# Performance work log

Hardware: AMD Instinct MI355X
Metric: run time of the kernel (lower is better)

Reference implementation:

```python
import jax, jax.numpy as jnp
import numpy as np

# config constants (from init_kwargs)
IMG_W = 800
IMG_H = 320
NUM_POINTS = 72
N_STRIPS = NUM_POINTS - 1
MAX_LANES = 4
REFINE_LAYERS = 3
CLS_W, REG_W, IOU_W = 2.0, 0.5, 2.0
ALPHA_NEG, ALPHA_POS, GAMMA = 0.1, 0.9, 2.0
LIOU_LEN = 15.0


def setup_inputs() -> dict:
    key = jax.random.key(0)
    k1, k2, k3, k4 = jax.random.split(key, 4)
    S, B, N, L, D = REFINE_LAYERS, 32, 2000, MAX_LANES, 2 + 4 + NUM_POINTS
    pred_fir = jax.random.uniform(k1, (S, B, N, D), dtype=jnp.float32)
    pred_sec = jax.random.uniform(k2, (S, B, N, D), dtype=jnp.float32)
    gt = jax.random.uniform(k3, (B, L, D), dtype=jnp.float32)
    gt = gt.at[..., 1].set(1.0)                    # all lanes valid
    # target offsets live in pixel coords; let some fall outside [0, IMG_W) to exercise invalid mask
    gt = gt.at[..., 6:].set(gt[..., 6:] * (IMG_W * 1.1) - 0.05 * IMG_W)
    diff = jax.random.uniform(k4, (S, N), dtype=jnp.float32)
    return {"predictions_fir": pred_fir, "predictions_sec": pred_sec,
            "gt_lane": gt, "diff": diff}


def _greedy_assign(cost):
    # cost: [N, L] -> matched prior row per target column, greedy without replacement
    N = cost.shape[0]
    def body(used, col):
        c = jnp.where(used, jnp.inf, col)
        r = jnp.argmin(c)
        return used.at[r].set(True), r
    _, rows = jax.lax.scan(body, jnp.zeros((N,), bool), cost.T)
    return rows  # [L] int32


def _assign_all(preds, gt):
    # preds: [S,B,N,D], gt: [B,L,D]; matching is under no_grad in the original
    p = jax.lax.stop_gradient(preds)
    t = jax.lax.stop_gradient(gt)
    score = jax.nn.softmax(p[..., :2], axis=-1)[..., 1]            # [S,B,N]
    geo = jnp.abs(p[..., :, None, 2:6] - t[None, :, None, :, 2:6]).sum(-1)   # [S,B,N,L]
    off = jnp.abs(p[..., :, None, 6:] - t[None, :, None, :, 6:] / (IMG_W - 1)).mean(-1)
    cost = geo + off - score[..., None]                            # [S,B,N,L]
    S, B, N, L = cost.shape
    rows = jax.vmap(_greedy_assign)(cost.reshape(S * B, N, L))
    return rows.reshape(S, B, L)


def _smooth_l1(d):
    ad = jnp.abs(d)
    return jnp.where(ad < 1.0, 0.5 * d * d, ad - 0.5)


def _branch_loss(preds, gt):
    # preds: [S,B,N,D], gt: [B,L,D] -> instance loss [N], last matched rows [L]
    S, B, N, _ = preds.shape
    L = gt.shape[1]
    rows = _assign_all(preds, gt)                                  # [S,B,L]

    # focal cls loss, per prior, summed over stages & batch
    cls_t = jax.nn.one_hot(rows, N, dtype=preds.dtype).sum(2)      # [S,B,N] 0/1
    logp = jax.nn.log_softmax(preds[..., :2], axis=-1)
    logpt = jnp.where(cls_t > 0, logp[..., 1], logp[..., 0])
    pt = jnp.exp(logpt)
    alpha_t = jnp.where(cls_t > 0, ALPHA_POS, ALPHA_NEG)
    cls_loss = (-alpha_t * (1.0 - pt) ** GAMMA * logpt).sum((0, 1)) / (B * REFINE_LAYERS)  # [N]

    # gather matched priors: [S,B,L,D]
    pm = jnp.take_along_axis(preds, rows[..., None], axis=2)
    tgt = gt[None]                                                 # [1,B,L,D]

    # smooth-L1 on (y, x, theta, length)
    sc = jnp.array([N_STRIPS, IMG_W - 1, 180.0, N_STRIPS], preds.dtype)
    d = pm[..., 2:6] * sc - tgt[..., 2:6] * sc
    reg_loss = (_smooth_l1(d).mean(-1) / L).sum((0, 1)) / (B * REFINE_LAYERS)  # [L]

    # line IoU loss on offsets
    rp = pm[..., 6:] * (IMG_W - 1)
    rt = jnp.broadcast_to(tgt[..., 6:], rp.shape)
    invalid = (rt < 0) | (rt >= IMG_W)
    ovr = jnp.minimum(rp + LIOU_LEN, rt + LIOU_LEN) - jnp.maximum(rp - LIOU_LEN, rt - LIOU_LEN)
    uni = jnp.maximum(rp + LIOU_LEN, rt + LIOU_LEN) - jnp.minimum(rp - LIOU_LEN, rt - LIOU_LEN)
    ovr = jnp.where(invalid, 0.0, ovr)
    uni = jnp.where(invalid, 0.0, uni)
    iou = ovr.sum(-1) / (uni.sum(-1) + 1e-9)                       # [S,B,L]
    iou_loss = ((1.0 - iou) / L).sum((0, 1)) / (B * REFINE_LAYERS) # [L]

    inst = cls_loss * CLS_W
    rows_last = rows[-1, -1]                                       # last stage, last image
    inst = inst.at[rows_last].add(reg_loss * REG_W + iou_loss * IOU_W)
    return inst


def reference(predictions_fir, predictions_sec, gt_lane, diff):
    loss_A = _branch_loss(predictions_fir, gt_lane)   # [N]
    loss_B = _branch_loss(predictions_sec, gt_lane)   # [N]
    diff_mean = diff.mean(0)                          # [N]
    delta = jax.lax.stop_gradient(jnp.median(loss_A - loss_B))
    loss_A = loss_A - delta / 2
    loss_B = loss_B + delta / 2
    total = jnp.sum((1.0 - diff_mean) * loss_A + diff_mean * loss_B)
    return total
```

## Files before the change

### kernel.cpp

```cpp
#include <hip/hip_runtime.h>
#include <math.h>

#define SDIM 3
#define BDIM 32
#define NPRI 2000
#define LDIM 4
#define DDIM 78
#define NOFF 72
#define NSB (SDIM * BDIM)
#define CHUNK 128
#define NCHUNK 16


__global__ __launch_bounds__(256) void prep_kernel(
    const float* __restrict__ gt, float* __restrict__ tgdiv,
    float* __restrict__ clsSum, float* __restrict__ corrws,
    float* __restrict__ regacc)
{
    int tid = blockIdx.x * 256 + threadIdx.x;
    if (tid < BDIM * 36 * 8) {
        int b = tid / 288, r = tid % 288, jj = r / 8, t = r % 8;
        int l = t >> 1, k = t & 1;
        tgdiv[tid] = gt[((size_t)b * LDIM + l) * DDIM + 6 + 2 * jj + k] / 799.0f;
    }
    if (tid < 2 * NPRI) { clsSum[tid] = 0.0f; corrws[tid] = 0.0f; }
    if (tid < 16) regacc[tid] = 0.0f;
}

__global__ __launch_bounds__(256) void cost_kernel(
    const float* __restrict__ predsA, const float* __restrict__ predsB,
    const float* __restrict__ gt, const float* __restrict__ tgdiv,
    float* __restrict__ costws, float* __restrict__ clsSum)
{
    const int chunk = blockIdx.x;
    const int sb = blockIdx.y;
    const int branch = blockIdx.z;
    const float* preds = branch ? predsB : predsA;
    const int bimg = sb % BDIM;
    const int tid = threadIdx.x;
    const int base_n = chunk * CHUNK;
    const int ntile = min(CHUNK, NPRI - base_n);

    __shared__ float tile[CHUNK * DDIM];

    {
        const float4* src = (const float4*)(preds + ((size_t)sb * NPRI + base_n) * DDIM);
        float4* dst = (float4*)tile;
        const int nf4 = ntile * DDIM / 4;
        for (int k = tid; k < nf4; k += 256) dst[k] = src[k];
    }
    __syncthreads();

    const int wv = tid >> 6, lane = tid & 63;
    const int i = wv * 32 + (lane >> 1);
    const int h = lane & 1;
    if (i >= ntile) return;
    const int n = base_n + i;
    const float* p = &tile[i * DDIM];

    const float* gtb = gt + (size_t)bimg * LDIM * DDIM;
    const float* tgb = tgdiv + (size_t)bimg * 288;

    float offs0 = 0.f, offs1 = 0.f, offs2 = 0.f, offs3 = 0.f;
    const int jj0 = h * 18;
#pragma unroll 6
    for (int jj = jj0; jj < jj0 + 18; ++jj) {
        float pv0 = p[6 + 2 * jj];
        float pv1 = p[7 + 2 * jj];
        const float* t8 = tgb + jj * 8;
        offs0 += fabsf(pv0 - t8[0]); offs0 += fabsf(pv1 - t8[1]);
        offs1 += fabsf(pv0 - t8[2]); offs1 += fabsf(pv1 - t8[3]);
        offs2 += fabsf(pv0 - t8[4]); offs2 += fabsf(pv1 - t8[5]);
        offs3 += fabsf(pv0 - t8[6]); offs3 += fabsf(pv1 - t8[7]);
    }
    offs0 += __shfl_xor(offs0, 1);
    offs1 += __shfl_xor(offs1, 1);
    offs2 += __shfl_xor(offs2, 1);
    offs3 += __shfl_xor(offs3, 1);

    if (h == 0) {
        float a = p[0], b1 = p[1];
        float m = fmaxf(a, b1);
        float ea = expf(a - m), eb = expf(b1 - m);
        float score = eb / (ea + eb);
        float g0 = p[2], g1 = p[3], g2 = p[4], g3 = p[5];
        float offs[4] = {offs0, offs1, offs2, offs3};
        float* cw = costws + ((size_t)(branch * NSB + sb) * LDIM) * NPRI + n;
#pragma unroll
        for (int l = 0; l < LDIM; ++l) {
            float geo = fabsf(g0 - gtb[l * DDIM + 2]) + fabsf(g1 - gtb[l * DDIM + 3])
                      + fabsf(g2 - gtb[l * DDIM + 4]) + fabsf(g3 - gtb[l * DDIM + 5]);
            cw[(size_t)l * NPRI] = geo + offs[l] / 72.0f - score;
        }
        float lse = m + logf(ea + eb);
        float logpt = a - lse;
        float pt = expf(logpt);
        float om = 1.0f - pt;
        atomicAdd(&clsSum[branch * NPRI + n], -(0.1f * om * om * logpt));
    }
}

__global__ __launch_bounds__(256) void assignloss_kernel(
    const float* __restrict__ predsA, const float* __restrict__ predsB,
    const float* __restrict__ gt, const float* __restrict__ costws,
    int* __restrict__ rowsws, float* __restrict__ regacc,
    float* __restrict__ corrws)
{
    const int sb = blockIdx.x, branch = blockIdx.y;
    const float* preds = branch ? predsB : predsA;
    const int tid = threadIdx.x;
    const int wv = tid >> 6, lane = tid & 63;
    const int bimg = sb % BDIM;

    __shared__ float cost[LDIM][NPRI];
    __shared__ float redv[4];
    __shared__ int   redi[4];
    __shared__ int   rows_lds[LDIM];

    const float4* src = (const float4*)(costws + (size_t)(branch * NSB + sb) * LDIM * NPRI);
    float4* dst = (float4*)&cost[0][0];
    for (int k = tid; k < LDIM * NPRI / 4; k += 256) dst[k] = src[k];
    __syncthreads();

    for (int l = 0; l < LDIM; ++l) {
        float bv = INFINITY; int bi = 0x7fffffff;
        for (int k = tid; k < NPRI; k += 256) {
            float v = cost[l][k];
            if (v < bv) { bv = v; bi = k; }
        }
#pragma unroll
        for (int off = 32; off > 0; off >>= 1) {
            float v2 = __shfl_down(bv, off);
            int   i2 = __shfl_down(bi, off);
            if (v2 < bv || (v2 == bv && i2 < bi)) { bv = v2; bi = i2; }
        }
        if (lane == 0) { redv[wv] = bv; redi[wv] = bi; }
        __syncthreads();
        if (tid == 0) {
            float fv = redv[0]; int fi = redi[0];
#pragma unroll
            for (int w = 1; w < 4; ++w)
                if (redv[w] < fv || (redv[w] == fv && redi[w] < fi)) { fv = redv[w]; fi = redi[w]; }
            rows_lds[l] = fi;
            cost[0][fi] = INFINITY; cost[1][fi] = INFINITY;
            cost[2][fi] = INFINITY; cost[3][fi] = INFINITY;
        }
        __syncthreads();
    }
    if (tid < LDIM && sb == NSB - 1) rowsws[branch * LDIM + tid] = rows_lds[tid];

    const int l = wv;
    const int row = rows_lds[l];
    const float* pm = preds + ((size_t)sb * NPRI + row) * DDIM;
    const float* tg = gt + ((size_t)bimg * LDIM + l) * DDIM;

    float osum = 0.f, usum = 0.f, rterm = 0.f;
    {
        float rp = pm[6 + lane] * 799.0f;
        float rt = tg[6 + lane];
        bool inv = (rt < 0.0f) || (rt >= 800.0f);
        float ov = fminf(rp, rt) - fmaxf(rp, rt) + 30.0f;
        float un = fmaxf(rp, rt) - fminf(rp, rt) + 30.0f;
        if (!inv) { osum += ov; usum += un; }
    }
    if (lane < 8) {
        float rp = pm[6 + lane + 64] * 799.0f;
        float rt = tg[6 + lane + 64];
        bool inv = (rt < 0.0f) || (rt >= 800.0f);
        float ov = fminf(rp, rt) - fmaxf(rp, rt) + 30.0f;
        float un = fmaxf(rp, rt) - fminf(rp, rt) + 30.0f;
        if (!inv) { osum += ov; usum += un; }
    }
    if (lane < 4) {
        const float scv[4] = {71.0f, 799.0f, 180.0f, 71.0f};
        float s = scv[lane];
        float d = pm[2 + lane] * s - tg[2 + lane] * s;
        float ad = fabsf(d);
        rterm = (ad < 1.0f) ? 0.5f * d * d : ad - 0.5f;
    }
#pragma unroll
    for (int off = 32; off > 0; off >>= 1) {
        osum += __shfl_down(osum, off);
        usum += __shfl_down(usum, off);
        rterm += __shfl_down(rterm, off);
    }
    if (lane == 0) {
        float iou = osum / (usum + 1e-9f);
        atomicAdd(&regacc[branch * 8 + l], (rterm / 4.0f) / 4.0f);
        atomicAdd(&regacc[branch * 8 + 4 + l], (1.0f - iou) / 4.0f);

        float a = pm[0], b1 = pm[1];
        float m = fmaxf(a, b1);
        float ea = expf(a - m), eb = expf(b1 - m);
        float lse = m + logf(ea + eb);
        float lp0 = a - lse, lp1 = b1 - lse;
        float pt0 = expf(lp0), pt1 = expf(lp1);
        float om0 = 1.0f - pt0, om1 = 1.0f - pt1;
        float neg = -(0.1f * om0 * om0 * lp0);
        float pos = -(0.9f * om1 * om1 * lp1);
        atomicAdd(&corrws[branch * NPRI + row], pos - neg);
    }
}

__global__ __launch_bounds__(1024) void final_kernel(
    const float* __restrict__ clsSum, const float* __restrict__ corrws,
    const float* __restrict__ regacc, const int* __restrict__ rowsws,
    const float* __restrict__ diff, float* __restrict__ out)
{
    __shared__ float instA[NPRI];
    __shared__ float instB[NPRI];
    __shared__ float sbuf[2048];
    __shared__ float red[1024];
    const int tid = threadIdx.x;

    for (int n = tid; n < NPRI; n += 1024) {
        float ia = (clsSum[n] + corrws[n]) * (2.0f / 96.0f);
        float ib = (clsSum[NPRI + n] + corrws[NPRI + n]) * (2.0f / 96.0f);
#pragma unroll
        for (int l = 0; l < 4; ++l) {
            if (rowsws[l] == n)
                ia += (regacc[l] / 96.0f) * 0.5f + (regacc[4 + l] / 96.0f) * 2.0f;
            if (rowsws[4 + l] == n)
                ib += (regacc[8 + l] / 96.0f) * 0.5f + (regacc[12 + l] / 96.0f) * 2.0f;
        }
        instA[n] = ia; instB[n] = ib;
        sbuf[n] = ia - ib;
    }
    if (tid < 2048 - NPRI) sbuf[NPRI + tid] = INFINITY;
    __syncthreads();

    for (int k = 2; k <= 2048; k <<= 1) {
        for (int j = k >> 1; j > 0; j >>= 1) {
            for (int i = tid; i < 2048; i += 1024) {
                int ixj = i ^ j;
                if (ixj > i) {
                    bool up = ((i & k) == 0);
                    float x = sbuf[i], y = sbuf[ixj];
                    if ((x > y) == up) { sbuf[i] = y; sbuf[ixj] = x; }
                }
            }
            __syncthreads();
        }
    }
    float delta = 0.5f * (sbuf[999] + sbuf[1000]);

    float acc = 0.0f;
    for (int n = tid; n < NPRI; n += 1024) {
        float dm = (diff[n] + diff[NPRI + n] + diff[2 * NPRI + n]) / 3.0f;
        acc += (1.0f - dm) * (instA[n] - 0.5f * delta)
             + dm * (instB[n] + 0.5f * delta);
    }
    red[tid] = acc;
    __syncthreads();
    for (int s = 512; s > 0; s >>= 1) {
        if (tid < s) red[tid] += red[tid + s];
        __syncthreads();
    }
    if (tid == 0) out[0] = red[0];
}

extern "C" void kernel_launch(void* const* d_in, const int* in_sizes, int n_in,
                              void* d_out, int out_size, void* d_ws, size_t ws_size,
                              hipStream_t stream)
{
    const float* predsA = (const float*)d_in[0];
    const float* predsB = (const float*)d_in[1];
    const float* gt     = (const float*)d_in[2];
    const float* diff   = (const float*)d_in[3];
    float* out = (float*)d_out;

    float* costws = (float*)d_ws;
    float* tgdiv  = costws + 2 * NSB * LDIM * NPRI;
    int*   rowsws = (int*)(tgdiv + BDIM * 36 * 8);
    float* clsSum = (float*)(rowsws + 8);
    float* corrws = clsSum + 2 * NPRI;
    float* regacc = corrws + 2 * NPRI;

    prep_kernel<<<40, 256, 0, stream>>>(gt, tgdiv, clsSum, corrws, regacc);

    dim3 g1(NCHUNK, NSB, 2);
    cost_kernel<<<g1, 256, 0, stream>>>(predsA, predsB, gt, tgdiv, costws, clsSum);

    dim3 g2(NSB, 2);
    assignloss_kernel<<<g2, 256, 0, stream>>>(predsA, predsB, gt, costws,
                                              rowsws, regacc, corrws);

    final_kernel<<<1, 1024, 0, stream>>>(clsSum, corrws, regacc, rowsws, diff, out);
}
```

Baseline: 202.2 us.

## Compute per-chunk top-4 candidates in cost kernel and merge greedily

The cost kernel now keeps each chunk's four lowest-cost candidates per target lane in registers and shared memory, instead of writing the full cost matrix to global memory. A small 64-thread merge kernel combines the chunk candidate lists and runs the greedy assignment over only the top-4 per lane. This removes the 2000x4 cost round trip and the serial argmin scans over shared memory. The prep kernel is replaced by a memset, and each thread now loads two whole prior rows as float4 vectors, which raises register pressure and gives strided, uncoalesced per-thread loads.

```diff
diff --git a/kernel.cpp b/kernel.cpp
--- a/kernel.cpp
+++ b/kernel.cpp
@@ -8,29 +8,23 @@
 #define DDIM 78
 #define NOFF 72
 #define NSB (SDIM * BDIM)
-#define CHUNK 128
-#define NCHUNK 16
-
-
-__global__ __launch_bounds__(256) void prep_kernel(
-    const float* __restrict__ gt, float* __restrict__ tgdiv,
-    float* __restrict__ clsSum, float* __restrict__ corrws,
-    float* __restrict__ regacc)
-{
-    int tid = blockIdx.x * 256 + threadIdx.x;
-    if (tid < BDIM * 36 * 8) {
-        int b = tid / 288, r = tid % 288, jj = r / 8, t = r % 8;
-        int l = t >> 1, k = t & 1;
-        tgdiv[tid] = gt[((size_t)b * LDIM + l) * DDIM + 6 + 2 * jj + k] / 799.0f;
-    }
-    if (tid < 2 * NPRI) { clsSum[tid] = 0.0f; corrws[tid] = 0.0f; }
-    if (tid < 16) regacc[tid] = 0.0f;
+#define PPB 512
+#define NCHUNK 4
+
+
+__device__ __forceinline__ void lexmin_bfly(float& v, int& i) {
+#pragma unroll
+    for (int off = 32; off > 0; off >>= 1) {
+        float v2 = __shfl_xor(v, off);
+        int   i2 = __shfl_xor(i, off);
+        if (v2 < v || (v2 == v && i2 < i)) { v = v2; i = i2; }
+    }
 }
 
 __global__ __launch_bounds__(256) void cost_kernel(
     const float* __restrict__ predsA, const float* __restrict__ predsB,
-    const float* __restrict__ gt, const float* __restrict__ tgdiv,
-    float* __restrict__ costws, float* __restrict__ clsSum)
+    const float* __restrict__ gt, float2* __restrict__ chunkTop,
+    float* __restrict__ clsSum)
 {
     const int chunk = blockIdx.x;
     const int sb = blockIdx.y;
@@ -38,167 +32,215 @@
     const float* preds = branch ? predsB : predsA;
     const int bimg = sb % BDIM;
     const int tid = threadIdx.x;
-    const int base_n = chunk * CHUNK;
-    const int ntile = min(CHUNK, NPRI - base_n);
-
-    __shared__ float tile[CHUNK * DDIM];
+    const int wv = tid >> 6, lane = tid & 63;
+
+    __shared__ float tgdiv[NOFF][4];
+    __shared__ float ggeo[LDIM][4];
+    __shared__ float wtv[4][LDIM][4];
+    __shared__ int   wti[4][LDIM][4];
+
+    if (tid < 256) { int j = tid >> 2, l = tid & 3;
+        tgdiv[j][l] = gt[((size_t)bimg * LDIM + l) * DDIM + 6 + j] / 799.0f; }
+    if (tid < 32)  { int k = 256 + tid; int j = k >> 2, l = k & 3;
+        tgdiv[j][l] = gt[((size_t)bimg * LDIM + l) * DDIM + 6 + j] / 799.0f; }
+    if (tid >= 32 && tid < 48) { int idx = tid - 32; int l = idx >> 2, d = idx & 3;
+        ggeo[l][d] = gt[((size_t)bimg * LDIM + l) * DDIM + 2 + d]; }
+    __syncthreads();
+
+    const int pr0 = chunk * PPB + 2 * tid;
+    const bool act = (pr0 < NPRI);
+
+    float a[2], bb[2], g[2][4];
+    float offs[2][4] = {{0.f,0.f,0.f,0.f},{0.f,0.f,0.f,0.f}};
+
+    if (act) {
+        const float4* b4 = (const float4*)(preds + ((size_t)sb * NPRI + pr0) * DDIM);
+#pragma unroll
+        for (int q = 0; q < 39; ++q) {
+            float4 v = b4[q];
+            float vv[4] = {v.x, v.y, v.z, v.w};
+#pragma unroll
+            for (int k = 0; k < 4; ++k) {
+                const int f = 4 * q + k;
+                const int p = (f >= DDIM) ? 1 : 0;
+                const int pos = f - DDIM * p;
+                float x = vv[k];
+                if (pos == 0) a[p] = x;
+                else if (pos == 1) bb[p] = x;
+                else if (pos < 6) g[p][pos - 2] = x;
+                else {
+                    const int j = pos - 6;
+#pragma unroll
+                    for (int l = 0; l < LDIM; ++l) offs[p][l] += fabsf(x - tgdiv[j][l]);
+                }
+            }
+        }
+    }
+
+    float c[2][LDIM];
+#pragma unroll
+    for (int p = 0; p < 2; ++p) {
+        if (act) {
+            float m = fmaxf(a[p], bb[p]);
+            float ea = expf(a[p] - m), eb = expf(bb[p] - m);
+            float score = eb / (ea + eb);
+#pragma unroll
+            for (int l = 0; l < LDIM; ++l) {
+                float geo = fabsf(g[p][0] - ggeo[l][0]) + fabsf(g[p][1] - ggeo[l][1])
+                          + fabsf(g[p][2] - ggeo[l][2]) + fabsf(g[p][3] - ggeo[l][3]);
+                c[p][l] = geo + offs[p][l] / 72.0f - score;
+            }
+            float lse = m + logf(ea + eb);
+            float logpt = a[p] - lse;
+            float pt = expf(logpt);
+            float om = 1.0f - pt;
+            atomicAdd(&clsSum[branch * NPRI + pr0 + p], -(0.1f * om * om * logpt));
+        } else {
+#pragma unroll
+            for (int l = 0; l < LDIM; ++l) c[p][l] = INFINITY;
+        }
+    }
+
+#pragma unroll
+    for (int l = 0; l < LDIM; ++l) {
+        float c0 = c[0][l], c1 = c[1][l];
+        int   i0 = pr0, i1 = pr0 + 1;
+        bool  m0 = !act, m1 = !act;
+#pragma unroll
+        for (int r = 0; r < 4; ++r) {
+            float lv; int li;
+            if (!m0 && (m1 || c0 <= c1)) { lv = c0; li = i0; }
+            else if (!m1)                { lv = c1; li = i1; }
+            else                         { lv = INFINITY; li = 0x7fffffff; }
+            lexmin_bfly(lv, li);
+            if (lane == 0) { wtv[wv][l][r] = lv; wti[wv][l][r] = li; }
+            if (li == i0) m0 = true;
+            if (li == i1) m1 = true;
+        }
+    }
+    __syncthreads();
 
     {
-        const float4* src = (const float4*)(preds + ((size_t)sb * NPRI + base_n) * DDIM);
-        float4* dst = (float4*)tile;
-        const int nf4 = ntile * DDIM / 4;
-        for (int k = tid; k < nf4; k += 256) dst[k] = src[k];
-    }
-    __syncthreads();
-
-    const int wv = tid >> 6, lane = tid & 63;
-    const int i = wv * 32 + (lane >> 1);
-    const int h = lane & 1;
-    if (i >= ntile) return;
-    const int n = base_n + i;
-    const float* p = &tile[i * DDIM];
-
-    const float* gtb = gt + (size_t)bimg * LDIM * DDIM;
-    const float* tgb = tgdiv + (size_t)bimg * 288;
-
-    float offs0 = 0.f, offs1 = 0.f, offs2 = 0.f, offs3 = 0.f;
-    const int jj0 = h * 18;
-#pragma unroll 6
-    for (int jj = jj0; jj < jj0 + 18; ++jj) {
-        float pv0 = p[6 + 2 * jj];
-        float pv1 = p[7 + 2 * jj];
-        const float* t8 = tgb + jj * 8;
-        offs0 += fabsf(pv0 - t8[0]); offs0 += fabsf(pv1 - t8[1]);
-        offs1 += fabsf(pv0 - t8[2]); offs1 += fabsf(pv1 - t8[3]);
-        offs2 += fabsf(pv0 - t8[4]); offs2 += fabsf(pv1 - t8[5]);
-        offs3 += fabsf(pv0 - t8[6]); offs3 += fabsf(pv1 - t8[7]);
-    }
-    offs0 += __shfl_xor(offs0, 1);
-    offs1 += __shfl_xor(offs1, 1);
-    offs2 += __shfl_xor(offs2, 1);
-    offs3 += __shfl_xor(offs3, 1);
-
-    if (h == 0) {
-        float a = p[0], b1 = p[1];
-        float m = fmaxf(a, b1);
-        float ea = expf(a - m), eb = expf(b1 - m);
-        float score = eb / (ea + eb);
-        float g0 = p[2], g1 = p[3], g2 = p[4], g3 = p[5];
-        float offs[4] = {offs0, offs1, offs2, offs3};
-        float* cw = costws + ((size_t)(branch * NSB + sb) * LDIM) * NPRI + n;
-#pragma unroll
-        for (int l = 0; l < LDIM; ++l) {
-            float geo = fabsf(g0 - gtb[l * DDIM + 2]) + fabsf(g1 - gtb[l * DDIM + 3])
-                      + fabsf(g2 - gtb[l * DDIM + 4]) + fabsf(g3 - gtb[l * DDIM + 5]);
-            cw[(size_t)l * NPRI] = geo + offs[l] / 72.0f - score;
-        }
-        float lse = m + logf(ea + eb);
-        float logpt = a - lse;
-        float pt = expf(logpt);
-        float om = 1.0f - pt;
-        atomicAdd(&clsSum[branch * NPRI + n], -(0.1f * om * om * logpt));
-    }
-}
-
-__global__ __launch_bounds__(256) void assignloss_kernel(
+        const int l = wv;
+        float v = INFINITY; int i = 0x7fffffff;
+        if (lane < 16) { v = wtv[lane >> 2][l][lane & 3]; i = wti[lane >> 2][l][lane & 3]; }
+        float outv[4]; int outi[4];
+#pragma unroll
+        for (int r = 0; r < 4; ++r) {
+            float lv = v; int li = i;
+            lexmin_bfly(lv, li);
+            outv[r] = lv; outi[r] = li;
+            if (li == i) v = INFINITY;
+        }
+        if (lane == 0) {
+            float2* dst = chunkTop + ((((size_t)(branch * NSB + sb)) * LDIM + l) * NCHUNK + chunk) * 4;
+#pragma unroll
+            for (int r = 0; r < 4; ++r) dst[r] = make_float2(outv[r], __int_as_float(outi[r]));
+        }
+    }
+}
+
+__global__ __launch_bounds__(64) void merge_kernel(
     const float* __restrict__ predsA, const float* __restrict__ predsB,
-    const float* __restrict__ gt, const float* __restrict__ costws,
+    const float* __restrict__ gt, const float2* __restrict__ chunkTop,
     int* __restrict__ rowsws, float* __restrict__ regacc,
     float* __restrict__ corrws)
 {
     const int sb = blockIdx.x, branch = blockIdx.y;
     const float* preds = branch ? predsB : predsA;
-    const int tid = threadIdx.x;
-    const int wv = tid >> 6, lane = tid & 63;
+    const int lane = threadIdx.x;
     const int bimg = sb % BDIM;
 
-    __shared__ float cost[LDIM][NPRI];
-    __shared__ float redv[4];
-    __shared__ int   redi[4];
+    __shared__ float tops_v[LDIM][4];
+    __shared__ int   tops_i[LDIM][4];
     __shared__ int   rows_lds[LDIM];
 
-    const float4* src = (const float4*)(costws + (size_t)(branch * NSB + sb) * LDIM * NPRI);
-    float4* dst = (float4*)&cost[0][0];
-    for (int k = tid; k < LDIM * NPRI / 4; k += 256) dst[k] = src[k];
-    __syncthreads();
-
     for (int l = 0; l < LDIM; ++l) {
-        float bv = INFINITY; int bi = 0x7fffffff;
-        for (int k = tid; k < NPRI; k += 256) {
-            float v = cost[l][k];
-            if (v < bv) { bv = v; bi = k; }
+        float v = INFINITY; int i = 0x7fffffff;
+        if (lane < 16) {
+            float2 e = chunkTop[((((size_t)(branch * NSB + sb)) * LDIM + l) * NCHUNK + (lane >> 2)) * 4 + (lane & 3)];
+            v = e.x; i = __float_as_int(e.y);
+        }
+#pragma unroll
+        for (int r = 0; r < 4; ++r) {
+            float lv = v; int li = i;
+            lexmin_bfly(lv, li);
+            if (lane == 0) { tops_v[l][r] = lv; tops_i[l][r] = li; }
+            if (li == i) v = INFINITY;
+        }
+    }
+    __syncthreads();
+
+    if (lane == 0) {
+        int used[LDIM];
+#pragma unroll
+        for (int l = 0; l < LDIM; ++l) {
+            int pick = tops_i[l][3];
+#pragma unroll
+            for (int r = 3; r >= 0; --r) {
+                int cand = tops_i[l][r];
+                bool ok = true;
+                for (int u = 0; u < l; ++u) ok = ok && (used[u] != cand);
+                if (ok) pick = cand;
+            }
+            used[l] = pick;
+            rows_lds[l] = pick;
+        }
+    }
+    __syncthreads();
+    if (sb == NSB - 1 && lane < LDIM) rowsws[branch * LDIM + lane] = rows_lds[lane];
+
+    for (int l = 0; l < LDIM; ++l) {
+        const int row = rows_lds[l];
+        const float* pm = preds + ((size_t)sb * NPRI + row) * DDIM;
+        const float* tg = gt + ((size_t)bimg * LDIM + l) * DDIM;
+
+        float osum = 0.f, usum = 0.f, rterm = 0.f;
+        {
+            float rp = pm[6 + lane] * 799.0f;
+            float rt = tg[6 + lane];
+            bool inv = (rt < 0.0f) || (rt >= 800.0f);
+            float ov = fminf(rp, rt) - fmaxf(rp, rt) + 30.0f;
+            float un = fmaxf(rp, rt) - fminf(rp, rt) + 30.0f;
+            if (!inv) { osum += ov; usum += un; }
+        }
+        if (lane < 8) {
+            float rp = pm[70 + lane] * 799.0f;
+            float rt = tg[70 + lane];
+            bool inv = (rt < 0.0f) || (rt >= 800.0f);
+            float ov = fminf(rp, rt) - fmaxf(rp, rt) + 30.0f;
+            float un = fmaxf(rp, rt) - fminf(rp, rt) + 30.0f;
+            if (!inv) { osum += ov; usum += un; }
+        }
+        if (lane < 4) {
+            const float scv[4] = {71.0f, 799.0f, 180.0f, 71.0f};
+            float s = scv[lane];
+            float d = pm[2 + lane] * s - tg[2 + lane] * s;
+            float ad = fabsf(d);
+            rterm = (ad < 1.0f) ? 0.5f * d * d : ad - 0.5f;
         }
 #pragma unroll
         for (int off = 32; off > 0; off >>= 1) {
-            float v2 = __shfl_down(bv, off);
-            int   i2 = __shfl_down(bi, off);
-            if (v2 < bv || (v2 == bv && i2 < bi)) { bv = v2; bi = i2; }
-        }
-        if (lane == 0) { redv[wv] = bv; redi[wv] = bi; }
-        __syncthreads();
-        if (tid == 0) {
-            float fv = redv[0]; int fi = redi[0];
-#pragma unroll
-            for (int w = 1; w < 4; ++w)
-                if (redv[w] < fv || (redv[w] == fv && redi[w] < fi)) { fv = redv[w]; fi = redi[w]; }
-            rows_lds[l] = fi;
-            cost[0][fi] = INFINITY; cost[1][fi] = INFINITY;
-            cost[2][fi] = INFINITY; cost[3][fi] = INFINITY;
-        }
-        __syncthreads();
-    }
-    if (tid < LDIM && sb == NSB - 1) rowsws[branch * LDIM + tid] = rows_lds[tid];
-
-    const int l = wv;
-    const int row = rows_lds[l];
-    const float* pm = preds + ((size_t)sb * NPRI + row) * DDIM;
-    const float* tg = gt + ((size_t)bimg * LDIM + l) * DDIM;
-
-    float osum = 0.f, usum = 0.f, rterm = 0.f;
-    {
-        float rp = pm[6 + lane] * 799.0f;
-        float rt = tg[6 + lane];
-        bool inv = (rt < 0.0f) || (rt >= 800.0f);
-        float ov = fminf(rp, rt) - fmaxf(rp, rt) + 30.0f;
-        float un = fmaxf(rp, rt) - fminf(rp, rt) + 30.0f;
-        if (!inv) { osum += ov; usum += un; }
-    }
-    if (lane < 8) {
-        float rp = pm[6 + lane + 64] * 799.0f;
-        float rt = tg[6 + lane + 64];
-        bool inv = (rt < 0.0f) || (rt >= 800.0f);
-        float ov = fminf(rp, rt) - fmaxf(rp, rt) + 30.0f;
-        float un = fmaxf(rp, rt) - fminf(rp, rt) + 30.0f;
-        if (!inv) { osum += ov; usum += un; }
-    }
-    if (lane < 4) {
-        const float scv[4] = {71.0f, 799.0f, 180.0f, 71.0f};
-        float s = scv[lane];
-        float d = pm[2 + lane] * s - tg[2 + lane] * s;
-        float ad = fabsf(d);
-        rterm = (ad < 1.0f) ? 0.5f * d * d : ad - 0.5f;
-    }
-#pragma unroll
-    for (int off = 32; off > 0; off >>= 1) {
-        osum += __shfl_down(osum, off);
-        usum += __shfl_down(usum, off);
-        rterm += __shfl_down(rterm, off);
-    }
-    if (lane == 0) {
-        float iou = osum / (usum + 1e-9f);
-        atomicAdd(&regacc[branch * 8 + l], (rterm / 4.0f) / 4.0f);
-        atomicAdd(&regacc[branch * 8 + 4 + l], (1.0f - iou) / 4.0f);
-
-        float a = pm[0], b1 = pm[1];
-        float m = fmaxf(a, b1);
-        float ea = expf(a - m), eb = expf(b1 - m);
-        float lse = m + logf(ea + eb);
-        float lp0 = a - lse, lp1 = b1 - lse;
-        float pt0 = expf(lp0), pt1 = expf(lp1);
-        float om0 = 1.0f - pt0, om1 = 1.0f - pt1;
-        float neg = -(0.1f * om0 * om0 * lp0);
-        float pos = -(0.9f * om1 * om1 * lp1);
-        atomicAdd(&corrws[branch * NPRI + row], pos - neg);
+            osum += __shfl_down(osum, off);
+            usum += __shfl_down(usum, off);
+            rterm += __shfl_down(rterm, off);
+        }
+        if (lane == 0) {
+            float iou = osum / (usum + 1e-9f);
+            atomicAdd(&regacc[branch * 8 + l], (rterm / 4.0f) / 4.0f);
+            atomicAdd(&regacc[branch * 8 + 4 + l], (1.0f - iou) / 4.0f);
+
+            float a = pm[0], b1 = pm[1];
+            float m = fmaxf(a, b1);
+            float ea = expf(a - m), eb = expf(b1 - m);
+            float lse = m + logf(ea + eb);
+            float lp0 = a - lse, lp1 = b1 - lse;
+            float pt0 = expf(lp0), pt1 = expf(lp1);
+            float om0 = 1.0f - pt0, om1 = 1.0f - pt1;
+            float neg = -(0.1f * om0 * om0 * lp0);
+            float pos = -(0.9f * om1 * om1 * lp1);
+            atomicAdd(&corrws[branch * NPRI + row], pos - neg);
+        }
     }
 }
 
@@ -269,21 +311,20 @@
     const float* diff   = (const float*)d_in[3];
     float* out = (float*)d_out;
 
-    float* costws = (float*)d_ws;
-    float* tgdiv  = costws + 2 * NSB * LDIM * NPRI;
-    int*   rowsws = (int*)(tgdiv + BDIM * 36 * 8);
-    float* clsSum = (float*)(rowsws + 8);
-    float* corrws = clsSum + 2 * NPRI;
-    float* regacc = corrws + 2 * NPRI;
-
-    prep_kernel<<<40, 256, 0, stream>>>(gt, tgdiv, clsSum, corrws, regacc);
+    float2* chunkTop = (float2*)d_ws;
+    float*  clsSum   = (float*)((char*)d_ws + 98304);
+    float*  corrws   = clsSum + 2 * NPRI;
+    float*  regacc   = corrws + 2 * NPRI;
+    int*    rowsws   = (int*)(regacc + 16);
+
+    hipMemsetAsync(clsSum, 0, (2 * NPRI + 2 * NPRI + 16) * sizeof(float), stream);
 
     dim3 g1(NCHUNK, NSB, 2);
-    cost_kernel<<<g1, 256, 0, stream>>>(predsA, predsB, gt, tgdiv, costws, clsSum);
+    cost_kernel<<<g1, 256, 0, stream>>>(predsA, predsB, gt, chunkTop, clsSum);
 
     dim3 g2(NSB, 2);
-    assignloss_kernel<<<g2, 256, 0, stream>>>(predsA, predsB, gt, costws,
-                                              rowsws, regacc, corrws);
+    merge_kernel<<<g2, 64, 0, stream>>>(predsA, predsB, gt, chunkTop,
+                                        rowsws, regacc, corrws);
 
     final_kernel<<<1, 1024, 0, stream>>>(clsSum, corrws, regacc, rowsws, diff, out);
 }
```

Result: slower. 265.1 us (+31.1%).
